# Kernel optimization log

Measured on AMD Instinct MI355X. Metric: run time of the kernel, lower is better.

The kernel has to match this reference:

```python
import jax, jax.numpy as jnp
import numpy as np

N_BATCH, CH, HW, KERNEL, STRIDE, VC = 8, 256, 96, 8, 3, 512


def setup_inputs() -> dict:
    key = jax.random.key(0)
    k0, k1, k2, k3 = jax.random.split(key, 4)
    kk = KERNEL * KERNEL
    x = jax.random.normal(k0, (N_BATCH, CH, HW, HW), dtype=jnp.float32)
    # 1x1 conv weight [vc, ch, 1, 1] stored as [vc, ch]
    conv_w = jax.random.normal(k1, (VC, CH), dtype=jnp.float32) * 0.05
    # integrate_mask_activation: Linear(ch+kk, 3ch) -> LeakyReLU(0.2) -> Linear(3ch, ch) -> Tanh
    W1 = jax.random.normal(k2, (3 * CH, CH + kk), dtype=jnp.float32) * 0.02
    b1 = jnp.zeros((3 * CH,), dtype=jnp.float32)
    W2 = jax.random.normal(k3, (CH, 3 * CH), dtype=jnp.float32) * 0.02
    b2 = jnp.zeros((CH,), dtype=jnp.float32)
    return {"x": x, "conv_w": conv_w, "W1": W1, "b1": b1, "W2": W2, "b2": b2}


def _unfold(x, k, s):
    # torch.nn.Unfold(kernel=(k,k), stride=s) -> patches [n, L, c, k, k]
    n, c, h, w = x.shape
    oh = (h - k) // s + 1
    ow = (w - k) // s + 1
    ih = (jnp.arange(oh) * s)[:, None] + jnp.arange(k)[None, :]  # [oh, k]
    iw = (jnp.arange(ow) * s)[:, None] + jnp.arange(k)[None, :]  # [ow, k]
    p = x[:, :, ih, :]          # [n, c, oh, k, w]
    p = p[:, :, :, :, iw]       # [n, c, oh, k, ow, k]
    p = p.transpose(0, 2, 4, 1, 3, 5)  # [n, oh, ow, c, k, k]
    return p.reshape(n, oh * ow, c, k, k), oh * ow


def reference(x, conv_w, W1, b1, W2, b2):
    k = KERNEL
    kk = k * k
    n, c, h, w = x.shape
    patches, L = _unfold(x, k, STRIDE)           # [n, L, c, k, k]
    N = n * L
    p = patches.reshape(N, c, k, k)

    # GenerateMask_2_0: normalized similarity via 1x1 conv
    x_norm = jnp.sqrt((p ** 2).sum(1))           # [N, k, k]
    w_norm = jnp.sqrt((conv_w ** 2).sum(1))      # [vc]
    y = jnp.einsum('nchw,vc->nvhw', p, conv_w)   # [N, vc, k, k]
    y = y / (x_norm[:, None, :, :] * w_norm[None, :, None, None])

    vc = conv_w.shape[0]
    y_flat = y.reshape(N, vc * kk)
    idx = jnp.argmax(y_flat, axis=1)                       # topk(k=1)
    max_sim = jnp.take_along_axis(y_flat, idx[:, None], axis=1)  # [N, 1]
    max_ch = idx // kk                                     # codebook index [N]
    col = idx % kk                                         # spatial index [N]

    rows = jnp.arange(N)
    sim_map_max = y.reshape(N, vc, kk)[rows, max_ch]       # [N, kk]
    max_act = p.reshape(N, c, kk)[rows, :, col]            # [N, c]
    vc_vec = conv_w[max_ch]                                # [N, c]
    integ = max_act * max_sim + vc_vec * (1.0 - max_sim)   # blend with codebook

    # integrate_mask_activation MLP
    inp = jnp.concatenate([integ, sim_map_max], axis=1)    # [N, c + kk]
    h1 = inp @ W1.T + b1
    h1 = jnp.where(h1 > 0, h1, 0.2 * h1)                   # LeakyReLU(0.2)
    out = jnp.tanh(h1 @ W2.T + b2)                         # [N, c]
    return out.reshape(n, L, c)
```

## Files before the change

kernel.cpp:

```cpp
#include <hip/hip_runtime.h>
#include <hip/hip_fp16.h>
#include <math.h>

#define NB 8
#define CHN 256
#define HWD 96
#define PIXN (HWD*HWD)
#define TOTPIX (NB*PIXN)
#define VCN 512
#define OHW 30
#define LPP (OHW*OHW)
#define NPATCH (NB*LPP)
#define INPD 320
#define HID 768
#define MTP 456

typedef unsigned short u16;
typedef __attribute__((ext_vector_type(8))) short bf16x8;
typedef __attribute__((ext_vector_type(8))) unsigned short us8;
typedef __attribute__((ext_vector_type(4))) float f32x4;

__device__ __forceinline__ float f4c(const float4 v, int i){
  return i==0 ? v.x : i==1 ? v.y : i==2 ? v.z : v.w;
}
__device__ __forceinline__ u16 bfrn(float f){
  unsigned u = __float_as_uint(f);
  return (u16)((u + 0x7fffu + ((u>>16)&1u)) >> 16);
}
__device__ __forceinline__ float bf2f(u16 h){
  return __uint_as_float(((unsigned)h)<<16);
}


template<int NS>
__global__ __launch_bounds__(64) void wsplit_k(const float* __restrict__ src,
                                               u16* __restrict__ dst, int K){
  const int rt = blockIdx.x, kk = blockIdx.y, kkc = gridDim.y;
  const int lane = threadIdx.x, qr = lane>>4, col = lane&15;
  const float* s = src + (size_t)(rt*16+col)*K + kk*32 + qr*8;
  us8 h1, h2, h3;
  #pragma unroll
  for (int j=0;j<8;j++){
    float a = s[j];
    u16 x1 = bfrn(a);  float r1 = a - bf2f(x1);
    u16 x2 = bfrn(r1); float r2 = r1 - bf2f(x2);
    h1[j]=x1; h2[j]=x2; h3[j]=bfrn(r2);
  }
  size_t base = ((size_t)(rt*kkc + kk)*NS)*512 + lane*8;
  *(us8*)&dst[base]     = h1;
  *(us8*)&dst[base+512] = h2;
  if (NS == 3) *(us8*)&dst[base+1024] = h3;
}

__global__ __launch_bounds__(256) void wnorm_k(const float* __restrict__ cw,
                                               float* __restrict__ invw){
  const int v = blockIdx.x*4 + (threadIdx.x>>6);
  const int lane = threadIdx.x & 63;
  const float4 a = *(const float4*)&cw[(size_t)v*CHN + lane*4];
  float s = fmaf(a.x,a.x, fmaf(a.y,a.y, fmaf(a.z,a.z, a.w*a.w)));
  #pragma unroll
  for (int off=32; off; off>>=1) s += __shfl_xor(s, off);
  if (lane==0) invw[v] = 1.0f/sqrtf(s);
}

__global__ __launch_bounds__(256,3) void gemm_z_k(
    const float* __restrict__ x, const u16* __restrict__ wf,
    const float* __restrict__ invw,
    float* __restrict__ pbest, int* __restrict__ pbidx,
    __half* __restrict__ zf){
  __shared__ __align__(16) u16 afr[2*8*3*512];
  __shared__ float ssq2[4][32];
  __shared__ float rv[32][4];
  __shared__ int   ri[32][4];
  const int t = threadIdx.x;
  const int wv = t>>6, lane = t&63;
  const int col = lane&15, qr = lane>>4;
  const size_t p0 = (size_t)blockIdx.x * 32;
  const int img = (int)(p0 / PIXN);
  const int pl0 = (int)(p0 % PIXN);

  {
    const int pi = t & 31, bq = t >> 5;
    const int fr = pi & 15, mt = pi >> 4;
    const float* xb = x + ((size_t)img*CHN)*PIXN + pl0 + pi;
    float s = 0.f;
    #pragma unroll
    for (int it=0; it<4; ++it){
      const int c0 = it*64 + bq*8;
      float xv[8];
      #pragma unroll
      for (int j=0;j<8;j++) xv[j] = xb[(size_t)(c0+j)*PIXN];
      us8 h1,h2,h3;
      #pragma unroll
      for (int j=0;j<8;j++){
        const float a = xv[j];
        s = fmaf(a,a,s);
        u16 x1 = bfrn(a);  float r1 = a - bf2f(x1);
        u16 x2 = bfrn(r1);
        h1[j]=x1; h2[j]=x2; h3[j]=bfrn(r1 - bf2f(x2));
      }
      const int kk = c0 >> 5, cq = (c0>>3)&3;
      u16* dstp = &afr[((mt*8+kk)*3)*512 + (cq*16+fr)*8];
      *(us8*)dstp        = h1;
      *(us8*)(dstp+512)  = h2;
      *(us8*)(dstp+1024) = h3;
    }
    s += __shfl_xor(s, 32);
    if (lane < 32) ssq2[wv][lane] = s;
  }
  __syncthreads();

  f32x4 acc[2][8];
  #pragma unroll
  for (int i=0;i<2;i++)
    #pragma unroll
    for (int j=0;j<8;j++) acc[i][j] = (f32x4){0.f,0.f,0.f,0.f};
  const size_t loff = (size_t)lane*8;
  const int loff16 = lane*8;
  for (int kk=0; kk<8; ++kk){
    bf16x8 a0[3], a1[3];
    {
      const int ab0 = (kk*3)*512 + loff16;
      const int ab1 = ((8+kk)*3)*512 + loff16;
      a0[0] = *(const bf16x8*)&afr[ab0];
      a0[1] = *(const bf16x8*)&afr[ab0+512];
      a0[2] = *(const bf16x8*)&afr[ab0+1024];
      a1[0] = *(const bf16x8*)&afr[ab1];
      a1[1] = *(const bf16x8*)&afr[ab1+512];
      a1[2] = *(const bf16x8*)&afr[ab1+1024];
    }
    #pragma unroll
    for (int h=0; h<2; ++h){
      bf16x8 bg[4][3];
      #pragma unroll
      for (int q=0;q<4;q++){
        const int ni = h*4+q;
        const size_t bb = (((size_t)(wv*8+ni)*8 + kk)*3)*512 + loff;
        bg[q][0] = *(const bf16x8*)&wf[bb];
        bg[q][1] = *(const bf16x8*)&wf[bb+512];
        bg[q][2] = *(const bf16x8*)&wf[bb+1024];
      }
      #pragma unroll
      for (int q=0;q<4;q++){
        const int ni = h*4+q;
        {
          f32x4 c = acc[0][ni];
          c = __builtin_amdgcn_mfma_f32_16x16x32_bf16(a0[0], bg[q][0], c, 0,0,0);
          c = __builtin_amdgcn_mfma_f32_16x16x32_bf16(a0[0], bg[q][1], c, 0,0,0);
          c = __builtin_amdgcn_mfma_f32_16x16x32_bf16(a0[1], bg[q][0], c, 0,0,0);
          c = __builtin_amdgcn_mfma_f32_16x16x32_bf16(a0[0], bg[q][2], c, 0,0,0);
          c = __builtin_amdgcn_mfma_f32_16x16x32_bf16(a0[1], bg[q][1], c, 0,0,0);
          c = __builtin_amdgcn_mfma_f32_16x16x32_bf16(a0[2], bg[q][0], c, 0,0,0);
          acc[0][ni] = c;
        }
        {
          f32x4 c = acc[1][ni];
          c = __builtin_amdgcn_mfma_f32_16x16x32_bf16(a1[0], bg[q][0], c, 0,0,0);
          c = __builtin_amdgcn_mfma_f32_16x16x32_bf16(a1[0], bg[q][1], c, 0,0,0);
          c = __builtin_amdgcn_mfma_f32_16x16x32_bf16(a1[1], bg[q][0], c, 0,0,0);
          c = __builtin_amdgcn_mfma_f32_16x16x32_bf16(a1[0], bg[q][2], c, 0,0,0);
          c = __builtin_amdgcn_mfma_f32_16x16x32_bf16(a1[1], bg[q][1], c, 0,0,0);
          c = __builtin_amdgcn_mfma_f32_16x16x32_bf16(a1[2], bg[q][0], c, 0,0,0);
          acc[1][ni] = c;
        }
      }
    }
  }

  float iw[8];
  #pragma unroll
  for (int ni=0;ni<8;ni++) iw[ni] = invw[wv*128 + ni*16 + col];
  #pragma unroll
  for (int mi=0;mi<2;mi++){
    #pragma unroll
    for (int r=0;r<4;r++){
      const int P = mi*16 + qr*4 + r;
      const float sq = ssq2[0][P] + ssq2[1][P] + ssq2[2][P] + ssq2[3][P];
      const float ip = rsqrtf(sq);
      float bz = -1e30f; int bvi = 0;
      #pragma unroll
      for (int ni=0;ni<8;ni++){
        const float z = f4c(*(const float4*)&acc[mi][ni], r) * ip * iw[ni];
        const int vv = wv*128 + ni*16 + col;
        zf[(p0+P)*VCN + vv] = __float2half(z);
        if (z > bz){ bz = z; bvi = vv; }
      }
      #pragma unroll
      for (int off=1; off<16; off<<=1){
        const float oz = __shfl_xor(bz, off);
        const int  oi = __shfl_xor(bvi, off);
        if (oz > bz || (oz == bz && oi < bvi)){ bz = oz; bvi = oi; }
      }
      if (col == 0){ rv[P][wv] = bz; ri[P][wv] = bvi; }
    }
  }
  __syncthreads();
  if (t < 32){
    float best = rv[t][0]; int bi = ri[t][0];
    #pragma unroll
    for (int s=1;s<4;s++){
      float z2 = rv[t][s]; int i2 = ri[t][s];
      if (z2 > best || (z2 == best && i2 < bi)){ best = z2; bi = i2; }
    }
    pbest[p0+t] = best; pbidx[p0+t] = bi;
  }
}

__global__ __launch_bounds__(64) void select_k(
    const float* __restrict__ x, const float* __restrict__ cw,
    const __half* __restrict__ zf,
    const float* __restrict__ pbest, const int* __restrict__ pbidx,
    u16* __restrict__ inpf){
  __shared__ float wlds[256];
  __shared__ float xcol[256];
  __shared__ float simv[64];
  const int q = blockIdx.x;
  const int lane = threadIdx.x;
  const int n = q / LPP, l = q % LPP;
  const int oy = l / OHW, ox = l % OHW;
  const int pl = (oy*3 + (lane >> 3))*HWD + (ox*3 + (lane & 7));
  const int p = n*PIXN + pl;
  const int rt = q >> 4, ql = q & 15;
  float val = pbest[p];
  int flat = pbidx[p]*64 + lane;
  #pragma unroll
  for (int off=32; off>0; off>>=1){
    float ov = __shfl_xor(val, off);
    int of = __shfl_xor(flat, off);
    if (ov > val || (ov == val && of < flat)){ val = ov; flat = of; }
  }
  const int mch = flat >> 6;
  const int pos = flat & 63;
  const float ms = val;
  *(float4*)&wlds[lane*4] = *(const float4*)&cw[(size_t)mch*CHN + lane*4];
  simv[lane] = __half2float(zf[(size_t)p*VCN + mch]);
  const int wpl = (oy*3 + (pos>>3))*HWD + (ox*3 + (pos&7));
  const float* xb = x + (size_t)n*CHN*PIXN + wpl;
  #pragma unroll
  for (int j=0;j<4;j++) xcol[lane*4+j] = xb[(size_t)(lane*4+j)*PIXN];
  __syncthreads();
  if (lane < 32){
    const int kk = lane >> 2, qr = lane & 3;
    const float om = 1.0f - ms;
    const int c0 = kk*32 + qr*8;
    us8 p1, p2;
    #pragma unroll
    for (int j=0;j<8;j++){
      float v = fmaf(xcol[c0+j], ms, wlds[c0+j]*om);
      u16 s1 = bfrn(v);
      p1[j] = s1; p2[j] = bfrn(v - bf2f(s1));
    }
    const size_t ob = ((size_t)(rt*10 + kk)*2)*512 + (qr*16 + ql)*8;
    *(us8*)&inpf[ob]     = p1;
    *(us8*)&inpf[ob+512] = p2;
  }
  if (lane < 16){
    const int s = lane >> 3, kk = 8 + ((lane >> 2) & 1), qr = lane & 3;
    us8 pv;
    #pragma unroll
    for (int j=0;j<8;j++){
      float v = simv[(kk-8)*32 + qr*8 + j];
      u16 s1 = bfrn(v);
      pv[j] = (s == 0) ? s1 : bfrn(v - bf2f(s1));
    }
    const size_t ob = ((size_t)(rt*10 + kk)*2 + s)*512 + (qr*16 + ql)*8;
    *(us8*)&inpf[ob] = pv;
  }
}

__global__ __launch_bounds__(256,2) void mlp1_k(
    const u16* __restrict__ af, const u16* __restrict__ bf,
    const float* __restrict__ bias, u16* __restrict__ h1f){
  const int kkc = INPD >> 5;
  const int t = threadIdx.x;
  const int n0 = blockIdx.x*128, m0 = blockIdx.y*128;
  const int lane = t&63, wv = t>>6;
  const int mq = wv&1, nq = wv>>1;
  const int col = lane&15, qr = lane>>4;
  const size_t loff = (size_t)lane*8;
  const int ptA0 = (m0>>4) + mq*4;
  const int ntB0 = (n0>>4) + nq*4;
  f32x4 acc[4][4];
  #pragma unroll
  for (int i=0;i<4;i++)
    #pragma unroll
    for (int j=0;j<4;j++) acc[i][j] = (f32x4){0.f,0.f,0.f,0.f};

  for (int kk=0; kk<kkc; kk++){
    bf16x8 a[4][2];
    #pragma unroll
    for (int mi=0;mi<4;mi++){
      const size_t ab = (((size_t)(ptA0+mi)*kkc + kk)*2)*512 + loff;
      a[mi][0] = *(const bf16x8*)&af[ab];
      a[mi][1] = *(const bf16x8*)&af[ab+512];
    }
    #pragma unroll
    for (int ni=0;ni<4;ni++){
      const size_t bb = (((size_t)(ntB0+ni)*kkc + kk)*2)*512 + loff;
      const bf16x8 b1 = *(const bf16x8*)&bf[bb];
      const bf16x8 b2 = *(const bf16x8*)&bf[bb+512];
      #pragma unroll
      for (int mi=0;mi<4;mi++){
        f32x4 c = acc[mi][ni];
        c = __builtin_amdgcn_mfma_f32_16x16x32_bf16(a[mi][0], b1, c, 0,0,0);
        c = __builtin_amdgcn_mfma_f32_16x16x32_bf16(a[mi][0], b2, c, 0,0,0);
        c = __builtin_amdgcn_mfma_f32_16x16x32_bf16(a[mi][1], b1, c, 0,0,0);
        acc[mi][ni] = c;
      }
    }
  }
  float bb4[4];
  #pragma unroll
  for (int ni=0;ni<4;ni++) bb4[ni] = bias[n0 + nq*64 + ni*16 + col];
  #pragma unroll
  for (int mi=0;mi<4;mi++){
    const int rt2 = (m0>>4) + mq*4 + mi;
    #pragma unroll
    for (int r=0;r<4;r++){
      #pragma unroll
      for (int ni=0;ni<4;ni++){
        float v = f4c(*(const float4*)&acc[mi][ni], r) + bb4[ni];
        v = v > 0.f ? v : 0.2f*v;
        u16 s1 = bfrn(v);
        u16 s2 = bfrn(v - bf2f(s1));
        const int kk2 = (n0>>5) + nq*2 + (ni>>1);
        const int qn = (ni&1)*2 + (col>>3);
        const size_t ob = ((size_t)(rt2*24 + kk2)*2)*512 + (qn*16 + qr*4 + r)*8 + (col&7);
        h1f[ob] = s1; h1f[ob+512] = s2;
      }
    }
  }
}

__global__ __launch_bounds__(256,2) void mlp2_k(
    const u16* __restrict__ af, const u16* __restrict__ bf,
    const float* __restrict__ bias, float* __restrict__ C){
  const int kkc = HID >> 5;
  const int t = threadIdx.x;
  const int n0 = blockIdx.x*128, m0 = blockIdx.y*128;
  const int lane = t&63, wv = t>>6;
  const int mq = wv&1, nq = wv>>1;
  const int col = lane&15, qr = lane>>4;
  const size_t loff = (size_t)lane*8;
  const int ptA0 = (m0>>4) + mq*4;
  const int ntB0 = (n0>>4) + nq*4;
  f32x4 acc[4][4];
  #pragma unroll
  for (int i=0;i<4;i++)
    #pragma unroll
    for (int j=0;j<4;j++) acc[i][j] = (f32x4){0.f,0.f,0.f,0.f};

  for (int kk=0; kk<kkc; kk++){
    bf16x8 a[4][2];
    #pragma unroll
    for (int mi=0;mi<4;mi++){
      const size_t ab = (((size_t)(ptA0+mi)*kkc + kk)*2)*512 + loff;
      a[mi][0] = *(const bf16x8*)&af[ab];
      a[mi][1] = *(const bf16x8*)&af[ab+512];
    }
    #pragma unroll
    for (int ni=0;ni<4;ni++){
      const size_t bb = (((size_t)(ntB0+ni)*kkc + kk)*2)*512 + loff;
      const bf16x8 b1 = *(const bf16x8*)&bf[bb];
      const bf16x8 b2 = *(const bf16x8*)&bf[bb+512];
      #pragma unroll
      for (int mi=0;mi<4;mi++){
        f32x4 c = acc[mi][ni];
        c = __builtin_amdgcn_mfma_f32_16x16x32_bf16(a[mi][0], b1, c, 0,0,0);
        c = __builtin_amdgcn_mfma_f32_16x16x32_bf16(a[mi][0], b2, c, 0,0,0);
        c = __builtin_amdgcn_mfma_f32_16x16x32_bf16(a[mi][1], b1, c, 0,0,0);
        acc[mi][ni] = c;
      }
    }
  }
  float bb4[4];
  #pragma unroll
  for (int ni=0;ni<4;ni++) bb4[ni] = bias[n0 + nq*64 + ni*16 + col];
  #pragma unroll
  for (int mi=0;mi<4;mi++){
    #pragma unroll
    for (int r=0;r<4;r++){
      const int row = m0 + mq*64 + mi*16 + qr*4 + r;
      if (row < NPATCH){
        #pragma unroll
        for (int ni=0;ni<4;ni++){
          float v = f4c(*(const float4*)&acc[mi][ni], r) + bb4[ni];
          C[(size_t)row*CHN + n0 + nq*64 + ni*16 + col] = tanhf(v);
        }
      }
    }
  }
}

extern "C" void kernel_launch(void* const* d_in, const int* in_sizes, int n_in,
                              void* d_out, int out_size, void* d_ws, size_t ws_size,
                              hipStream_t stream){
  const float* x  = (const float*)d_in[0];
  const float* cw = (const float*)d_in[1];
  const float* W1 = (const float*)d_in[2];
  const float* b1 = (const float*)d_in[3];
  const float* W2 = (const float*)d_in[4];
  const float* b2 = (const float*)d_in[5];
  float* out = (float*)d_out;
  float* ws = (float*)d_ws;
  float* invw  = ws;
  float* pbest = invw + VCN;
  int*   pbidx = (int*)(pbest + TOTPIX);
  u16*   wf    = (u16*)(pbidx + TOTPIX);
  u16*   w1f   = wf + (size_t)32*8*3*512;
  u16*   w2f   = w1f + (size_t)48*10*2*512;
  u16*   inpf  = w2f + (size_t)16*24*2*512;
  __half* zf   = (__half*)(inpf + (size_t)MTP*10*2*512);
  u16*   h1f   = (u16*)zf;

  wsplit_k<3><<<dim3(VCN/16, CHN/32),64,0,stream>>>(cw, wf, CHN);
  wsplit_k<2><<<dim3(HID/16, INPD/32),64,0,stream>>>(W1, w1f, INPD);
  wsplit_k<2><<<dim3(CHN/16, HID/32),64,0,stream>>>(W2, w2f, HID);
  wnorm_k<<<VCN/4,256,0,stream>>>(cw, invw);
  gemm_z_k<<<TOTPIX/32,256,0,stream>>>(x, wf, invw, pbest, pbidx, zf);
  select_k<<<NPATCH,64,0,stream>>>(x, cw, zf, pbest, pbidx, inpf);
  mlp1_k<<<dim3(HID/128, (NPATCH+127)/128),256,0,stream>>>(inpf, w1f, b1, h1f);
  mlp2_k<<<dim3(CHN/128, (NPATCH+127)/128),256,0,stream>>>(h1f, w2f, b2, out);
}
```

Measured before the change: 329.7 us.

## Prefetch codebook fragments in registers and merge weight-prep kernels into one launch

The z-GEMM main loop now double-buffers the codebook B fragments in registers. Next-k fragments for the first four column tiles load while MFMAs run on the current ones, and the second half's loads are issued ahead of the first half's math. Launch bounds drop from 3 to 2 so the extra live registers fit, at the cost of possible lower occupancy. The three weight-split kernels and the weight-norm kernel are folded into a single prep_k launch that dispatches on block index, removing three launches.

After: 367.9 us. 11.6% more time.

```diff
diff --git a/kernel.cpp b/kernel.cpp
--- a/kernel.cpp
+++ b/kernel.cpp
@@ -33,10 +33,10 @@
 
 
 template<int NS>
-__global__ __launch_bounds__(64) void wsplit_k(const float* __restrict__ src,
-                                               u16* __restrict__ dst, int K){
-  const int rt = blockIdx.x, kk = blockIdx.y, kkc = gridDim.y;
-  const int lane = threadIdx.x, qr = lane>>4, col = lane&15;
+__device__ __forceinline__ void split_body(const float* __restrict__ src,
+                                           u16* __restrict__ dst, int K,
+                                           int rt, int kk, int kkc, int lane){
+  const int qr = lane>>4, col = lane&15;
   const float* s = src + (size_t)(rt*16+col)*K + kk*32 + qr*8;
   us8 h1, h2, h3;
   #pragma unroll
@@ -52,18 +52,35 @@
   if (NS == 3) *(us8*)&dst[base+1024] = h3;
 }
 
-__global__ __launch_bounds__(256) void wnorm_k(const float* __restrict__ cw,
-                                               float* __restrict__ invw){
-  const int v = blockIdx.x*4 + (threadIdx.x>>6);
-  const int lane = threadIdx.x & 63;
-  const float4 a = *(const float4*)&cw[(size_t)v*CHN + lane*4];
+__global__ __launch_bounds__(64) void prep_k(
+    const float* __restrict__ cw, const float* __restrict__ W1,
+    const float* __restrict__ W2, u16* __restrict__ wf,
+    u16* __restrict__ w1f, u16* __restrict__ w2f, float* __restrict__ invw){
+  int b = blockIdx.x;
+  const int lane = threadIdx.x;
+  if (b < 256){ split_body<3>(cw, wf, CHN, b>>3, b&7, 8, lane); return; }
+  b -= 256;
+  if (b < 480){ split_body<2>(W1, w1f, INPD, b/10, b%10, 10, lane); return; }
+  b -= 480;
+  if (b < 384){ split_body<2>(W2, w2f, HID, b/24, b%24, 24, lane); return; }
+  b -= 384;
+  const float4 a = *(const float4*)&cw[(size_t)b*CHN + lane*4];
   float s = fmaf(a.x,a.x, fmaf(a.y,a.y, fmaf(a.z,a.z, a.w*a.w)));
   #pragma unroll
   for (int off=32; off; off>>=1) s += __shfl_xor(s, off);
-  if (lane==0) invw[v] = 1.0f/sqrtf(s);
-}
-
-__global__ __launch_bounds__(256,3) void gemm_z_k(
+  if (lane==0) invw[b] = 1.0f/sqrtf(s);
+}
+
+__device__ __forceinline__ void mfma6(f32x4& c, const bf16x8* A, const bf16x8* B){
+  c = __builtin_amdgcn_mfma_f32_16x16x32_bf16(A[0], B[0], c, 0,0,0);
+  c = __builtin_amdgcn_mfma_f32_16x16x32_bf16(A[0], B[1], c, 0,0,0);
+  c = __builtin_amdgcn_mfma_f32_16x16x32_bf16(A[1], B[0], c, 0,0,0);
+  c = __builtin_amdgcn_mfma_f32_16x16x32_bf16(A[0], B[2], c, 0,0,0);
+  c = __builtin_amdgcn_mfma_f32_16x16x32_bf16(A[1], B[1], c, 0,0,0);
+  c = __builtin_amdgcn_mfma_f32_16x16x32_bf16(A[2], B[0], c, 0,0,0);
+}
+
+__global__ __launch_bounds__(256,2) void gemm_z_k(
     const float* __restrict__ x, const u16* __restrict__ wf,
     const float* __restrict__ invw,
     float* __restrict__ pbest, int* __restrict__ pbidx,
@@ -117,6 +134,15 @@
     for (int j=0;j<8;j++) acc[i][j] = (f32x4){0.f,0.f,0.f,0.f};
   const size_t loff = (size_t)lane*8;
   const int loff16 = lane*8;
+
+  bf16x8 P[4][3], Q[4][3];
+  #pragma unroll
+  for (int q=0;q<4;q++){
+    const size_t bb = (((size_t)(wv*8+q)*8 + 0)*3)*512 + loff;
+    P[q][0] = *(const bf16x8*)&wf[bb];
+    P[q][1] = *(const bf16x8*)&wf[bb+512];
+    P[q][2] = *(const bf16x8*)&wf[bb+1024];
+  }
   for (int kk=0; kk<8; ++kk){
     bf16x8 a0[3], a1[3];
     {
@@ -130,40 +156,30 @@
       a1[2] = *(const bf16x8*)&afr[ab1+1024];
     }
     #pragma unroll
-    for (int h=0; h<2; ++h){
-      bf16x8 bg[4][3];
+    for (int q=0;q<4;q++){
+      const size_t bb = (((size_t)(wv*8+4+q)*8 + kk)*3)*512 + loff;
+      Q[q][0] = *(const bf16x8*)&wf[bb];
+      Q[q][1] = *(const bf16x8*)&wf[bb+512];
+      Q[q][2] = *(const bf16x8*)&wf[bb+1024];
+    }
+    #pragma unroll
+    for (int q=0;q<4;q++){
+      mfma6(acc[0][q], a0, P[q]);
+      mfma6(acc[1][q], a1, P[q]);
+    }
+    if (kk < 7){
       #pragma unroll
       for (int q=0;q<4;q++){
-        const int ni = h*4+q;
-        const size_t bb = (((size_t)(wv*8+ni)*8 + kk)*3)*512 + loff;
-        bg[q][0] = *(const bf16x8*)&wf[bb];
-        bg[q][1] = *(const bf16x8*)&wf[bb+512];
-        bg[q][2] = *(const bf16x8*)&wf[bb+1024];
-      }
-      #pragma unroll
-      for (int q=0;q<4;q++){
-        const int ni = h*4+q;
-        {
-          f32x4 c = acc[0][ni];
-          c = __builtin_amdgcn_mfma_f32_16x16x32_bf16(a0[0], bg[q][0], c, 0,0,0);
-          c = __builtin_amdgcn_mfma_f32_16x16x32_bf16(a0[0], bg[q][1], c, 0,0,0);
-          c = __builtin_amdgcn_mfma_f32_16x16x32_bf16(a0[1], bg[q][0], c, 0,0,0);
-          c = __builtin_amdgcn_mfma_f32_16x16x32_bf16(a0[0], bg[q][2], c, 0,0,0);
-          c = __builtin_amdgcn_mfma_f32_16x16x32_bf16(a0[1], bg[q][1], c, 0,0,0);
-          c = __builtin_amdgcn_mfma_f32_16x16x32_bf16(a0[2], bg[q][0], c, 0,0,0);
-          acc[0][ni] = c;
-        }
-        {
-          f32x4 c = acc[1][ni];
-          c = __builtin_amdgcn_mfma_f32_16x16x32_bf16(a1[0], bg[q][0], c, 0,0,0);
-          c = __builtin_amdgcn_mfma_f32_16x16x32_bf16(a1[0], bg[q][1], c, 0,0,0);
-          c = __builtin_amdgcn_mfma_f32_16x16x32_bf16(a1[1], bg[q][0], c, 0,0,0);
-          c = __builtin_amdgcn_mfma_f32_16x16x32_bf16(a1[0], bg[q][2], c, 0,0,0);
-          c = __builtin_amdgcn_mfma_f32_16x16x32_bf16(a1[1], bg[q][1], c, 0,0,0);
-          c = __builtin_amdgcn_mfma_f32_16x16x32_bf16(a1[2], bg[q][0], c, 0,0,0);
-          acc[1][ni] = c;
-        }
-      }
+        const size_t bb = (((size_t)(wv*8+q)*8 + (kk+1))*3)*512 + loff;
+        P[q][0] = *(const bf16x8*)&wf[bb];
+        P[q][1] = *(const bf16x8*)&wf[bb+512];
+        P[q][2] = *(const bf16x8*)&wf[bb+1024];
+      }
+    }
+    #pragma unroll
+    for (int q=0;q<4;q++){
+      mfma6(acc[0][4+q], a0, Q[q]);
+      mfma6(acc[1][4+q], a1, Q[q]);
     }
   }
 
@@ -174,15 +190,15 @@
   for (int mi=0;mi<2;mi++){
     #pragma unroll
     for (int r=0;r<4;r++){
-      const int P = mi*16 + qr*4 + r;
-      const float sq = ssq2[0][P] + ssq2[1][P] + ssq2[2][P] + ssq2[3][P];
+      const int P2 = mi*16 + qr*4 + r;
+      const float sq = ssq2[0][P2] + ssq2[1][P2] + ssq2[2][P2] + ssq2[3][P2];
       const float ip = rsqrtf(sq);
       float bz = -1e30f; int bvi = 0;
       #pragma unroll
       for (int ni=0;ni<8;ni++){
         const float z = f4c(*(const float4*)&acc[mi][ni], r) * ip * iw[ni];
         const int vv = wv*128 + ni*16 + col;
-        zf[(p0+P)*VCN + vv] = __float2half(z);
+        zf[(p0+P2)*VCN + vv] = __float2half(z);
         if (z > bz){ bz = z; bvi = vv; }
       }
       #pragma unroll
@@ -191,7 +207,7 @@
         const int  oi = __shfl_xor(bvi, off);
         if (oz > bz || (oz == bz && oi < bvi)){ bz = oz; bvi = oi; }
       }
-      if (col == 0){ rv[P][wv] = bz; ri[P][wv] = bvi; }
+      if (col == 0){ rv[P2][wv] = bz; ri[P2][wv] = bvi; }
     }
   }
   __syncthreads();
@@ -413,10 +429,7 @@
   __half* zf   = (__half*)(inpf + (size_t)MTP*10*2*512);
   u16*   h1f   = (u16*)zf;
 
-  wsplit_k<3><<<dim3(VCN/16, CHN/32),64,0,stream>>>(cw, wf, CHN);
-  wsplit_k<2><<<dim3(HID/16, INPD/32),64,0,stream>>>(W1, w1f, INPD);
-  wsplit_k<2><<<dim3(CHN/16, HID/32),64,0,stream>>>(W2, w2f, HID);
-  wnorm_k<<<VCN/4,256,0,stream>>>(cw, invw);
+  prep_k<<<1632,64,0,stream>>>(cw, W1, W2, wf, w1f, w2f, invw);
   gemm_z_k<<<TOTPIX/32,256,0,stream>>>(x, wf, invw, pbest, pbidx, zf);
   select_k<<<NPATCH,64,0,stream>>>(x, cw, zf, pbest, pbidx, inpf);
   mlp1_k<<<dim3(HID/128, (NPATCH+127)/128),256,0,stream>>>(inpf, w1f, b1, h1f);
```
